# Optimization experiments

Hardware: AMD Instinct MI355X
Metric: run time of the kernel (lower is better)

Reference implementation:

```python
import jax, jax.numpy as jnp
import numpy as np

N_NODES = 50000
N_EDGES = 800000
N_GRAPHS = 128
IN_CH, HIDDEN, OUT_CH = 16, 64, 2


def gcn_conv(x, src, dst, W, b, n_nodes):
    """GCNConv: add self-loops, sym-normalized adjacency scatter-add, linear."""
    h = x @ W  # [N, H]
    loop = jnp.arange(n_nodes, dtype=src.dtype)
    s = jnp.concatenate([src, loop])  # [E+N]
    d = jnp.concatenate([dst, loop])
    deg = jax.ops.segment_sum(jnp.ones_like(d, dtype=h.dtype), d, num_segments=n_nodes)
    dinv = jnp.where(deg > 0, jax.lax.rsqrt(deg), 0.0)  # deg^{-1/2}
    norm = dinv[s] * dinv[d]  # [E+N]
    msg = h[s] * norm[:, None]  # gather + scale, [E+N, H]
    out = jax.ops.segment_sum(msg, d, num_segments=n_nodes)  # scatter-add
    return out + b


def global_mean_pool(x, batch, n_graphs):
    sums = jax.ops.segment_sum(x, batch, num_segments=n_graphs)
    cnts = jax.ops.segment_sum(jnp.ones((x.shape[0],), x.dtype), batch, num_segments=n_graphs)
    return sums / jnp.maximum(cnts, 1.0)[:, None]


def setup_inputs() -> dict:
    key = jax.random.key(0)
    ks = jax.random.split(key, 10)
    x = jax.random.normal(ks[0], (N_NODES, IN_CH), dtype=jnp.float32)
    edge_index = jax.random.randint(ks[1], (2, N_EDGES), 0, N_NODES, dtype=jnp.int64)
    batch = jnp.sort(jax.random.randint(ks[2], (N_NODES,), 0, N_GRAPHS, dtype=jnp.int64))
    def glorot(k, shp):
        lim = float(np.sqrt(6.0 / (shp[0] + shp[1])))
        return jax.random.uniform(k, shp, jnp.float32, -lim, lim)
    W1 = glorot(ks[3], (IN_CH, HIDDEN))
    b1 = jnp.zeros((HIDDEN,), jnp.float32)
    W2 = glorot(ks[4], (HIDDEN, HIDDEN))
    b2 = jnp.zeros((HIDDEN,), jnp.float32)
    Wc = glorot(ks[5], (HIDDEN, OUT_CH))
    bc = jnp.zeros((OUT_CH,), jnp.float32)
    return {"x": x, "edge_index": edge_index, "batch": batch,
            "W1": W1, "b1": b1, "W2": W2, "b2": b2, "Wc": Wc, "bc": bc}


def reference(x, edge_index, batch, W1, b1, W2, b2, Wc, bc):
    src, dst = edge_index[0], edge_index[1]
    n = x.shape[0]
    h = jax.nn.relu(gcn_conv(x, src, dst, W1, b1, n))
    # dropout p=0.3 is identity in eval mode
    h = jax.nn.relu(gcn_conv(h, src, dst, W2, b2, n))
    g = global_mean_pool(h, batch, N_GRAPHS)  # [G, H]
    return g @ Wc + bc  # [G, out_channels]
```

## Files before the change

### kernel.cpp

```cpp
#include <hip/hip_runtime.h>
#include <hip/hip_bf16.h>

#define N_NODES 50000
#define N_EDGES 800000
#define N_GRAPHS 128
#define IN_CH 16
#define HIDDEN 64
#define OUT_CH 2

#define BSHIFT 7
#define BNODES 128
#define NB ((N_NODES + BNODES - 1) / BNODES)
#define ECHUNK 4096
#define EB ((N_EDGES + ECHUNK - 1) / ECHUNK)
#define SLEN (NB * EB)
#define SCHUNK 1024
#define NSB ((SLEN + SCHUNK - 1) / SCHUNK)
#define MAXK 12
#define WT_LD 68

__device__ __forceinline__ float bf2f(unsigned short u) {
    return __uint_as_float(((unsigned)u) << 16);
}


__global__ void bucket_hist_kernel(const int* __restrict__ dst, int* __restrict__ bh,
                                   float* __restrict__ sums, float* __restrict__ cntg) {
    __shared__ int lh[NB];
    int t = threadIdx.x;
    if (blockIdx.x == 0) {
        for (int i = t; i < N_GRAPHS * HIDDEN; i += 256) sums[i] = 0.0f;
        if (t < N_GRAPHS) cntg[t] = 0.0f;
    }
    for (int i = t; i < NB; i += 256) lh[i] = 0;
    __syncthreads();
    int base = blockIdx.x * ECHUNK;
    for (int i = t; i < ECHUNK; i += 256) {
        int e = base + i;
        if (e < N_EDGES) {
            int d = dst[e];
            if ((unsigned)d < N_NODES) atomicAdd(&lh[d >> BSHIFT], 1);
        }
    }
    __syncthreads();
    for (int i = t; i < NB; i += 256) bh[i * EB + blockIdx.x] = lh[i];
}

__global__ void scan_part_kernel(const int* __restrict__ a, int* __restrict__ bsum) {
    __shared__ int s[256];
    int t = threadIdx.x;
    int ebase = blockIdx.x * SCHUNK + t * 4;
    int v = 0;
    if (ebase + 3 < SLEN) {
        int4 c = *(const int4*)&a[ebase];
        v = c.x + c.y + c.z + c.w;
    } else {
        for (int k = 0; k < 4; k++) {
            int i = ebase + k;
            if (i < SLEN) v += a[i];
        }
    }
    s[t] = v;
    __syncthreads();
    for (int off = 128; off > 0; off >>= 1) {
        if (t < off) s[t] += s[t + off];
        __syncthreads();
    }
    if (t == 0) bsum[blockIdx.x] = s[0];
}

__global__ void scan_apply_kernel(const int* __restrict__ a, const int* __restrict__ bsum,
                                  int* __restrict__ boff) {
    __shared__ int sb[256];
    __shared__ int st[256];
    int t = threadIdx.x;
    sb[t] = (t < NSB) ? bsum[t] : 0;
    __syncthreads();
    for (int off = 1; off < 256; off <<= 1) {
        int u = (t >= off) ? sb[t - off] : 0;
        __syncthreads();
        sb[t] += u;
        __syncthreads();
    }
    int blockOff = (blockIdx.x > 0) ? sb[blockIdx.x - 1] : 0;

    int ebase = blockIdx.x * SCHUNK + t * 4;
    int c0 = 0, c1 = 0, c2 = 0, c3 = 0;
    bool full = (ebase + 3 < SLEN);
    if (full) {
        int4 c = *(const int4*)&a[ebase];
        c0 = c.x; c1 = c.y; c2 = c.z; c3 = c.w;
    } else {
        if (ebase < SLEN) c0 = a[ebase];
        if (ebase + 1 < SLEN) c1 = a[ebase + 1];
        if (ebase + 2 < SLEN) c2 = a[ebase + 2];
    }
    int tsum = c0 + c1 + c2 + c3;
    st[t] = tsum;
    __syncthreads();
    for (int off = 1; off < 256; off <<= 1) {
        int u = (t >= off) ? st[t - off] : 0;
        __syncthreads();
        st[t] += u;
        __syncthreads();
    }
    int p = blockOff + st[t] - tsum;
    if (full) {
        int4 o;
        o.x = p; o.y = p + c0; o.z = p + c0 + c1; o.w = p + c0 + c1 + c2;
        *(int4*)&boff[ebase] = o;
    } else {
        if (ebase < SLEN) boff[ebase] = p;
        if (ebase + 1 < SLEN) boff[ebase + 1] = p + c0;
        if (ebase + 2 < SLEN) boff[ebase + 2] = p + c0 + c1;
        if (ebase + 3 < SLEN) boff[ebase + 3] = p + c0 + c1 + c2;
    }
}

__global__ void bucket_scatter_kernel(const int* __restrict__ src, const int* __restrict__ dst,
                                      const int* __restrict__ boff, int2* __restrict__ pairs) {
    __shared__ int lcnt[NB];
    __shared__ int goff[NB];
    int t = threadIdx.x;
    for (int i = t; i < NB; i += 256) {
        lcnt[i] = 0;
        goff[i] = boff[i * EB + blockIdx.x];
    }
    __syncthreads();
    int base = blockIdx.x * ECHUNK;
    for (int i = t; i < ECHUNK; i += 256) {
        int e = base + i;
        if (e < N_EDGES) {
            int d = dst[e];
            if ((unsigned)d < N_NODES) {
                int b = d >> BSHIFT;
                int r = atomicAdd(&lcnt[b], 1);
                int2 p;
                p.x = src[e];
                p.y = d;
                pairs[goff[b] + r] = p;
            }
        }
    }
}

__global__ void bucket_csr_kernel(const int2* __restrict__ pairs, const int* __restrict__ boff,
                                  int* __restrict__ csr, int* __restrict__ rowptr,
                                  int* __restrict__ cnt_node, float* __restrict__ dinv) {
    __shared__ int lcnt[BNODES];
    __shared__ int ls[BNODES];
    __shared__ int lrow[BNODES];
    int b = blockIdx.x;
    int t = threadIdx.x;
    if (t < BNODES) lcnt[t] = 0;
    __syncthreads();
    int bstart = boff[b * EB];
    int bend = (b + 1 < NB) ? boff[(b + 1) * EB] : N_EDGES;
    int K = bend - bstart;
    int myn[MAXK], myr[MAXK], mys[MAXK];
#pragma unroll
    for (int k = 0; k < MAXK; k++) {
        int i = k * 256 + t;
        if (i < K) {
            int2 p = pairs[bstart + i];
            int nl = p.y & (BNODES - 1);
            mys[k] = p.x;
            myn[k] = nl;
            myr[k] = atomicAdd(&lcnt[nl], 1);
        }
    }
    __syncthreads();
    if (t < BNODES) ls[t] = lcnt[t];
    __syncthreads();
    for (int off = 1; off < BNODES; off <<= 1) {
        int u = (t >= off && t < BNODES) ? ls[t - off] : 0;
        __syncthreads();
        if (t < BNODES) ls[t] += u;
        __syncthreads();
    }
    if (t < BNODES) {
        int ex = ls[t] - lcnt[t];
        lrow[t] = ex;
        int n = b * BNODES + t;
        if (n < N_NODES) {
            rowptr[n] = bstart + ex;
            cnt_node[n] = lcnt[t];
            dinv[n] = rsqrtf((float)(lcnt[t] + 1));
        }
    }
    __syncthreads();
#pragma unroll
    for (int k = 0; k < MAXK; k++) {
        int i = k * 256 + t;
        if (i < K) csr[bstart + lrow[myn[k]] + myr[k]] = mys[k];
    }
}


__global__ void fused_l1_kernel(const float* __restrict__ x, const int* __restrict__ csr_src,
                                const int* __restrict__ rowptr, const int* __restrict__ cnt,
                                const float* __restrict__ dinv, const float* __restrict__ W,
                                const float* __restrict__ b, __hip_bfloat16* __restrict__ h) {
    __shared__ float sWT[HIDDEN * 20];
    __shared__ float sx[16 * IN_CH];
    int t = threadIdx.x;
    for (int i = t; i < IN_CH * HIDDEN; i += 256) {
        int k = i >> 6, c = i & 63;
        sWT[c * 20 + k] = W[i];
    }

    int n0 = blockIdx.x * 16;
    int w = t >> 6;
    int lane = t & 63;
    int e4 = lane >> 2;
    int cc = (lane & 3) * 4;
    for (int q = 0; q < 4; q++) {
        int row = w * 4 + q;
        int n = n0 + row;
        if (n >= N_NODES) break;
        int len = cnt[n];
        int start = rowptr[n];
        float4 acc = make_float4(0.f, 0.f, 0.f, 0.f);
        for (int i = e4; i < len; i += 16) {
            int s = csr_src[start + i];
            float dv = dinv[s];
            float4 xv = *(const float4*)&x[s * IN_CH + cc];
            acc.x += dv * xv.x; acc.y += dv * xv.y; acc.z += dv * xv.z; acc.w += dv * xv.w;
        }
#pragma unroll
        for (int m = 4; m <= 32; m <<= 1) {
            acc.x += __shfl_xor(acc.x, m, 64);
            acc.y += __shfl_xor(acc.y, m, 64);
            acc.z += __shfl_xor(acc.z, m, 64);
            acc.w += __shfl_xor(acc.w, m, 64);
        }
        if (lane < 4) {
            float dn = dinv[n];
            float4 xs = *(const float4*)&x[n * IN_CH + cc];
            float4 v;
            v.x = dn * acc.x + dn * dn * xs.x;
            v.y = dn * acc.y + dn * dn * xs.y;
            v.z = dn * acc.z + dn * dn * xs.z;
            v.w = dn * acc.w + dn * dn * xs.w;
            *(float4*)&sx[row * IN_CH + cc] = v;
        }
    }
    __syncthreads();

    int r = w;
    int c = t & 63;
    float bias = b[c];
#pragma unroll
    for (int nb = 0; nb < 4; nb++) {
        int row = nb * 4 + r;
        int n = n0 + row;
        if (n >= N_NODES) continue;
        float acc = bias;
#pragma unroll
        for (int k4 = 0; k4 < IN_CH; k4 += 4) {
            float4 a = *(const float4*)&sx[row * IN_CH + k4];
            float4 wv = *(const float4*)&sWT[c * 20 + k4];
            acc += a.x * wv.x + a.y * wv.y + a.z * wv.z + a.w * wv.w;
        }
        float v = acc > 0.0f ? acc : 0.0f;
        h[n * HIDDEN + c] = __float2bfloat16(dinv[n] * v);
    }
}


__global__ void fused_l2_kernel(const __hip_bfloat16* __restrict__ h, const int* __restrict__ csr_src,
                                const int* __restrict__ rowptr, const int* __restrict__ cnt,
                                const float* __restrict__ dinv, const float* __restrict__ W,
                                const float* __restrict__ b, const int* __restrict__ batch,
                                float* __restrict__ sums, float* __restrict__ cntg) {
    __shared__ float sWT[HIDDEN * WT_LD];
    __shared__ float sagg[16 * HIDDEN];
    __shared__ float sred[4 * HIDDEN];
    int t = threadIdx.x;
    for (int i = t; i < HIDDEN * HIDDEN; i += 256) {
        int k = i >> 6, c = i & 63;
        sWT[c * WT_LD + k] = W[i];
    }

    int n0 = blockIdx.x * 16;
    int w = t >> 6;
    int lane = t & 63;
    int e4 = lane >> 4;
    int cc = (lane & 15) * 4;
    const unsigned short* hu = (const unsigned short*)h;

    for (int q = 0; q < 4; q++) {
        int row = w * 4 + q;
        int n = n0 + row;
        if (n >= N_NODES) break;
        int len = cnt[n];
        int start = rowptr[n];
        float4 acc = make_float4(0.f, 0.f, 0.f, 0.f);
        int i = e4;
        for (; i + 4 < len; i += 8) {
            int s0 = csr_src[start + i];
            int s1 = csr_src[start + i + 4];
            ushort4 a = *(const ushort4*)&hu[s0 * HIDDEN + cc];
            ushort4 bq = *(const ushort4*)&hu[s1 * HIDDEN + cc];
            acc.x += bf2f(a.x) + bf2f(bq.x);
            acc.y += bf2f(a.y) + bf2f(bq.y);
            acc.z += bf2f(a.z) + bf2f(bq.z);
            acc.w += bf2f(a.w) + bf2f(bq.w);
        }
        for (; i < len; i += 4) {
            int s0 = csr_src[start + i];
            ushort4 a = *(const ushort4*)&hu[s0 * HIDDEN + cc];
            acc.x += bf2f(a.x);
            acc.y += bf2f(a.y);
            acc.z += bf2f(a.z);
            acc.w += bf2f(a.w);
        }
        acc.x += __shfl_xor(acc.x, 16, 64);
        acc.y += __shfl_xor(acc.y, 16, 64);
        acc.z += __shfl_xor(acc.z, 16, 64);
        acc.w += __shfl_xor(acc.w, 16, 64);
        acc.x += __shfl_xor(acc.x, 32, 64);
        acc.y += __shfl_xor(acc.y, 32, 64);
        acc.z += __shfl_xor(acc.z, 32, 64);
        acc.w += __shfl_xor(acc.w, 32, 64);
        if (lane < 16) {
            ushort4 sv = *(const ushort4*)&hu[n * HIDDEN + cc];
            float dn = dinv[n];
            float4 v;
            v.x = dn * (acc.x + bf2f(sv.x));
            v.y = dn * (acc.y + bf2f(sv.y));
            v.z = dn * (acc.z + bf2f(sv.z));
            v.w = dn * (acc.w + bf2f(sv.w));
            *(float4*)&sagg[row * HIDDEN + cc] = v;
        }
    }
    __syncthreads();

    int r = w;
    int c = t & 63;
    float bias = b[c];
    float vout[4];
#pragma unroll
    for (int nb = 0; nb < 4; nb++) {
        int row = nb * 4 + r;
        int n = n0 + row;
        vout[nb] = 0.0f;
        if (n >= N_NODES) continue;
        float acc = bias;
#pragma unroll
        for (int k4 = 0; k4 < HIDDEN; k4 += 4) {
            float4 a = *(const float4*)&sagg[row * HIDDEN + k4];
            float4 wv = *(const float4*)&sWT[c * WT_LD + k4];
            acc += a.x * wv.x + a.y * wv.y + a.z * wv.z + a.w * wv.w;
        }
        vout[nb] = acc > 0.0f ? acc : 0.0f;
    }
    __syncthreads();

#pragma unroll
    for (int nb = 0; nb < 4; nb++) {
        int row = nb * 4 + r;
        if (n0 + row < N_NODES) sagg[row * HIDDEN + c] = vout[nb];
    }
    __syncthreads();

    int nlast = n0 + 15;
    if (nlast >= N_NODES) nlast = N_NODES - 1;
    int glo = batch[n0];
    int ghi = batch[nlast];
    if (glo == ghi) {
        float p = 0.0f;
#pragma unroll
        for (int q = 0; q < 4; q++) {
            int row = 4 * r + q;
            if (n0 + row < N_NODES) p += sagg[row * HIDDEN + c];
        }
        sred[r * HIDDEN + c] = p;
        __syncthreads();
        if (r == 0) {
            float v = sred[c] + sred[HIDDEN + c] + sred[2 * HIDDEN + c] + sred[3 * HIDDEN + c];
            atomicAdd(&sums[glo * HIDDEN + c], v);
            if (c == 0) atomicAdd(&cntg[glo], (float)(nlast - n0 + 1));
        }
    } else {
        int gcur = -1;
        float acc = 0.0f, ccnt = 0.0f;
        for (int q = 0; q < 4; q++) {
            int row = 4 * r + q;
            int n = n0 + row;
            if (n >= N_NODES) break;
            int g = batch[n];
            if ((unsigned)g >= N_GRAPHS) continue;
            if (g != gcur) {
                if (gcur >= 0) {
                    atomicAdd(&sums[gcur * HIDDEN + c], acc);
                    if (c == 0) atomicAdd(&cntg[gcur], ccnt);
                }
                gcur = g;
                acc = 0.0f;
                ccnt = 0.0f;
            }
            acc += sagg[row * HIDDEN + c];
            ccnt += 1.0f;
        }
        if (gcur >= 0) {
            atomicAdd(&sums[gcur * HIDDEN + c], acc);
            if (c == 0) atomicAdd(&cntg[gcur], ccnt);
        }
    }
}


__global__ void head_kernel(const float* __restrict__ sums, const float* __restrict__ cntg,
                            const float* __restrict__ Wc, const float* __restrict__ bc,
                            float* __restrict__ out) {
    int t = blockIdx.x * blockDim.x + threadIdx.x;
    if (t >= N_GRAPHS * OUT_CH) return;
    int g = t >> 1;
    int o = t & 1;
    float inv = 1.0f / fmaxf(cntg[g], 1.0f);
    float acc = bc[o];
#pragma unroll
    for (int k = 0; k < HIDDEN; k++) acc += sums[g * HIDDEN + k] * inv * Wc[k * OUT_CH + o];
    out[t] = acc;
}


extern "C" void kernel_launch(void* const* d_in, const int* in_sizes, int n_in,
                              void* d_out, int out_size, void* d_ws, size_t ws_size,
                              hipStream_t stream) {
    const float* x  = (const float*)d_in[0];
    const int* ei   = (const int*)d_in[1];
    const int* bat  = (const int*)d_in[2];
    const float* W1 = (const float*)d_in[3];
    const float* b1 = (const float*)d_in[4];
    const float* W2 = (const float*)d_in[5];
    const float* b2 = (const float*)d_in[6];
    const float* Wc = (const float*)d_in[7];
    const float* bc = (const float*)d_in[8];
    float* out = (float*)d_out;

    const int* src = ei;
    const int* dst = ei + N_EDGES;

    char* ws = (char*)d_ws;
    size_t off = 0;
    auto carve = [&](size_t nbytes) {
        char* p = ws + off;
        off += (nbytes + 255) & ~(size_t)255;
        return p;
    };
    float* sums     = (float*)carve(N_GRAPHS * HIDDEN * sizeof(float));
    float* cntg     = (float*)carve(N_GRAPHS * sizeof(float));
    int*   bh       = (int*)carve((size_t)SLEN * sizeof(int));
    int*   bsum     = (int*)carve(NSB * sizeof(int));
    int*   boff     = (int*)carve((size_t)SLEN * sizeof(int));
    int2*  pairs    = (int2*)carve((size_t)N_EDGES * sizeof(int2));
    int*   csr      = (int*)carve((size_t)N_EDGES * sizeof(int));
    int*   rowptr   = (int*)carve(N_NODES * sizeof(int));
    int*   cnt_node = (int*)carve(N_NODES * sizeof(int));
    float* dinv     = (float*)carve(N_NODES * sizeof(float));
    __hip_bfloat16* bufA = (__hip_bfloat16*)carve((size_t)N_NODES * HIDDEN * sizeof(__hip_bfloat16));
    (void)ws_size;

    const int node16Blk = (N_NODES + 15) / 16;

    bucket_hist_kernel<<<EB, 256, 0, stream>>>(dst, bh, sums, cntg);
    scan_part_kernel<<<NSB, 256, 0, stream>>>(bh, bsum);
    scan_apply_kernel<<<NSB, 256, 0, stream>>>(bh, bsum, boff);
    bucket_scatter_kernel<<<EB, 256, 0, stream>>>(src, dst, boff, pairs);
    bucket_csr_kernel<<<NB, 256, 0, stream>>>(pairs, boff, csr, rowptr, cnt_node, dinv);

    fused_l1_kernel<<<node16Blk, 256, 0, stream>>>(x, csr, rowptr, cnt_node, dinv, W1, b1, bufA);
    fused_l2_kernel<<<node16Blk, 256, 0, stream>>>(bufA, csr, rowptr, cnt_node, dinv, W2, b2,
                                                   bat, sums, cntg);
    head_kernel<<<1, 256, 0, stream>>>(sums, cntg, Wc, bc, out);
}
```

Baseline: 183.4 us.

## Use bf16 MFMA for layer-2 linear and simplify pooling reduction

Layer 2's 16x64x64 dense transform moves from scalar FP32 dot products in shared memory to two bf16 MFMA 16x16x32 instructions per wave. Both the aggregated features and the weights are stored in shared memory as bf16 with a padded stride. The pooling step now reduces directly from the MFMA output registers with shuffles, which drops the extra shared buffer and two barriers. The gather loop is also unrolled to four edges per iteration. The N_NODES bound checks are removed, which relies on 50000 being divisible by 16, and rounding the aggregate and weights to bf16 lowers precision.

```diff
diff --git a/kernel.cpp b/kernel.cpp
--- a/kernel.cpp
+++ b/kernel.cpp
@@ -17,10 +17,18 @@
 #define SCHUNK 1024
 #define NSB ((SLEN + SCHUNK - 1) / SCHUNK)
 #define MAXK 12
-#define WT_LD 68
+#define WT1_LD 18
+#define AGG_LD 72
+
+typedef __attribute__((ext_vector_type(8))) short bf16x8;
+typedef __attribute__((ext_vector_type(4))) float f32x4;
 
 __device__ __forceinline__ float bf2f(unsigned short u) {
     return __uint_as_float(((unsigned)u) << 16);
+}
+__device__ __forceinline__ unsigned short f2bf(float f) {
+    __hip_bfloat16 h = __float2bfloat16(f);
+    return *reinterpret_cast<unsigned short*>(&h);
 }
 
 
@@ -201,19 +209,20 @@
                                 const int* __restrict__ rowptr, const int* __restrict__ cnt,
                                 const float* __restrict__ dinv, const float* __restrict__ W,
                                 const float* __restrict__ b, __hip_bfloat16* __restrict__ h) {
-    __shared__ float sWT[HIDDEN * 20];
+    __shared__ float sWT[HIDDEN * WT1_LD];
     __shared__ float sx[16 * IN_CH];
     int t = threadIdx.x;
     for (int i = t; i < IN_CH * HIDDEN; i += 256) {
         int k = i >> 6, c = i & 63;
-        sWT[c * 20 + k] = W[i];
+        sWT[c * WT1_LD + k] = W[i];
     }
 
     int n0 = blockIdx.x * 16;
     int w = t >> 6;
     int lane = t & 63;
-    int e4 = lane >> 2;
+    int e16 = lane >> 2;
     int cc = (lane & 3) * 4;
+
     for (int q = 0; q < 4; q++) {
         int row = w * 4 + q;
         int n = n0 + row;
@@ -221,11 +230,12 @@
         int len = cnt[n];
         int start = rowptr[n];
         float4 acc = make_float4(0.f, 0.f, 0.f, 0.f);
-        for (int i = e4; i < len; i += 16) {
+        for (int i = e16; i < len; i += 16) {
             int s = csr_src[start + i];
             float dv = dinv[s];
             float4 xv = *(const float4*)&x[s * IN_CH + cc];
-            acc.x += dv * xv.x; acc.y += dv * xv.y; acc.z += dv * xv.z; acc.w += dv * xv.w;
+            acc.x += dv * xv.x; acc.y += dv * xv.y;
+            acc.z += dv * xv.z; acc.w += dv * xv.w;
         }
 #pragma unroll
         for (int m = 4; m <= 32; m <<= 1) {
@@ -255,14 +265,15 @@
         int row = nb * 4 + r;
         int n = n0 + row;
         if (n >= N_NODES) continue;
-        float acc = bias;
+        float acch = bias;
 #pragma unroll
         for (int k4 = 0; k4 < IN_CH; k4 += 4) {
             float4 a = *(const float4*)&sx[row * IN_CH + k4];
-            float4 wv = *(const float4*)&sWT[c * 20 + k4];
-            acc += a.x * wv.x + a.y * wv.y + a.z * wv.z + a.w * wv.w;
-        }
-        float v = acc > 0.0f ? acc : 0.0f;
+            float2 w0 = *(const float2*)&sWT[c * WT1_LD + k4];
+            float2 w1 = *(const float2*)&sWT[c * WT1_LD + k4 + 2];
+            acch += a.x * w0.x + a.y * w0.y + a.z * w1.x + a.w * w1.y;
+        }
+        float v = acch > 0.0f ? acch : 0.0f;
         h[n * HIDDEN + c] = __float2bfloat16(dinv[n] * v);
     }
 }
@@ -273,13 +284,12 @@
                                 const float* __restrict__ dinv, const float* __restrict__ W,
                                 const float* __restrict__ b, const int* __restrict__ batch,
                                 float* __restrict__ sums, float* __restrict__ cntg) {
-    __shared__ float sWT[HIDDEN * WT_LD];
-    __shared__ float sagg[16 * HIDDEN];
-    __shared__ float sred[4 * HIDDEN];
+    __shared__ unsigned short sW[HIDDEN * AGG_LD];
+    __shared__ unsigned short sagg[16 * AGG_LD];
     int t = threadIdx.x;
     for (int i = t; i < HIDDEN * HIDDEN; i += 256) {
         int k = i >> 6, c = i & 63;
-        sWT[c * WT_LD + k] = W[i];
+        sW[c * AGG_LD + k] = f2bf(W[i]);
     }
 
     int n0 = blockIdx.x * 16;
@@ -292,28 +302,31 @@
     for (int q = 0; q < 4; q++) {
         int row = w * 4 + q;
         int n = n0 + row;
-        if (n >= N_NODES) break;
         int len = cnt[n];
         int start = rowptr[n];
         float4 acc = make_float4(0.f, 0.f, 0.f, 0.f);
         int i = e4;
-        for (; i + 4 < len; i += 8) {
+        for (; i + 12 < len; i += 16) {
             int s0 = csr_src[start + i];
             int s1 = csr_src[start + i + 4];
-            ushort4 a = *(const ushort4*)&hu[s0 * HIDDEN + cc];
-            ushort4 bq = *(const ushort4*)&hu[s1 * HIDDEN + cc];
-            acc.x += bf2f(a.x) + bf2f(bq.x);
-            acc.y += bf2f(a.y) + bf2f(bq.y);
-            acc.z += bf2f(a.z) + bf2f(bq.z);
-            acc.w += bf2f(a.w) + bf2f(bq.w);
+            int s2 = csr_src[start + i + 8];
+            int s3 = csr_src[start + i + 12];
+            ushort4 a0 = *(const ushort4*)&hu[s0 * HIDDEN + cc];
+            ushort4 a1 = *(const ushort4*)&hu[s1 * HIDDEN + cc];
+            ushort4 a2 = *(const ushort4*)&hu[s2 * HIDDEN + cc];
+            ushort4 a3 = *(const ushort4*)&hu[s3 * HIDDEN + cc];
+            acc.x += (bf2f(a0.x) + bf2f(a1.x)) + (bf2f(a2.x) + bf2f(a3.x));
+            acc.y += (bf2f(a0.y) + bf2f(a1.y)) + (bf2f(a2.y) + bf2f(a3.y));
+            acc.z += (bf2f(a0.z) + bf2f(a1.z)) + (bf2f(a2.z) + bf2f(a3.z));
+            acc.w += (bf2f(a0.w) + bf2f(a1.w)) + (bf2f(a2.w) + bf2f(a3.w));
         }
         for (; i < len; i += 4) {
             int s0 = csr_src[start + i];
-            ushort4 a = *(const ushort4*)&hu[s0 * HIDDEN + cc];
-            acc.x += bf2f(a.x);
-            acc.y += bf2f(a.y);
-            acc.z += bf2f(a.z);
-            acc.w += bf2f(a.w);
+            ushort4 a0 = *(const ushort4*)&hu[s0 * HIDDEN + cc];
+            acc.x += bf2f(a0.x);
+            acc.y += bf2f(a0.y);
+            acc.z += bf2f(a0.z);
+            acc.w += bf2f(a0.w);
         }
         acc.x += __shfl_xor(acc.x, 16, 64);
         acc.y += __shfl_xor(acc.y, 16, 64);
@@ -326,86 +339,54 @@
         if (lane < 16) {
             ushort4 sv = *(const ushort4*)&hu[n * HIDDEN + cc];
             float dn = dinv[n];
-            float4 v;
-            v.x = dn * (acc.x + bf2f(sv.x));
-            v.y = dn * (acc.y + bf2f(sv.y));
-            v.z = dn * (acc.z + bf2f(sv.z));
-            v.w = dn * (acc.w + bf2f(sv.w));
-            *(float4*)&sagg[row * HIDDEN + cc] = v;
-        }
-    }
-    __syncthreads();
-
-    int r = w;
-    int c = t & 63;
-    float bias = b[c];
-    float vout[4];
-#pragma unroll
-    for (int nb = 0; nb < 4; nb++) {
-        int row = nb * 4 + r;
-        int n = n0 + row;
-        vout[nb] = 0.0f;
-        if (n >= N_NODES) continue;
-        float acc = bias;
-#pragma unroll
-        for (int k4 = 0; k4 < HIDDEN; k4 += 4) {
-            float4 a = *(const float4*)&sagg[row * HIDDEN + k4];
-            float4 wv = *(const float4*)&sWT[c * WT_LD + k4];
-            acc += a.x * wv.x + a.y * wv.y + a.z * wv.z + a.w * wv.w;
-        }
-        vout[nb] = acc > 0.0f ? acc : 0.0f;
-    }
-    __syncthreads();
-
-#pragma unroll
-    for (int nb = 0; nb < 4; nb++) {
-        int row = nb * 4 + r;
-        if (n0 + row < N_NODES) sagg[row * HIDDEN + c] = vout[nb];
-    }
-    __syncthreads();
-
-    int nlast = n0 + 15;
-    if (nlast >= N_NODES) nlast = N_NODES - 1;
+            ushort4 o;
+            o.x = f2bf(dn * (acc.x + bf2f(sv.x)));
+            o.y = f2bf(dn * (acc.y + bf2f(sv.y)));
+            o.z = f2bf(dn * (acc.z + bf2f(sv.z)));
+            o.w = f2bf(dn * (acc.w + bf2f(sv.w)));
+            *(ushort4*)&sagg[row * AGG_LD + cc] = o;
+        }
+    }
+    __syncthreads();
+
+    int quad = lane >> 4;
+    int col = lane & 15;
+    int cch = w * 16 + col;
+    bf16x8 a0 = *(const bf16x8*)&sagg[col * AGG_LD + quad * 8];
+    bf16x8 a1 = *(const bf16x8*)&sagg[col * AGG_LD + 32 + quad * 8];
+    bf16x8 b0 = *(const bf16x8*)&sW[cch * AGG_LD + quad * 8];
+    bf16x8 b1 = *(const bf16x8*)&sW[cch * AGG_LD + 32 + quad * 8];
+    f32x4 d = {0.f, 0.f, 0.f, 0.f};
+    d = __builtin_amdgcn_mfma_f32_16x16x32_bf16(a0, b0, d, 0, 0, 0);
+    d = __builtin_amdgcn_mfma_f32_16x16x32_bf16(a1, b1, d, 0, 0, 0);
+    float bias = b[cch];
+    float v[4];
+#pragma unroll
+    for (int r = 0; r < 4; r++) {
+        float z = d[r] + bias;
+        v[r] = z > 0.0f ? z : 0.0f;
+    }
+
     int glo = batch[n0];
-    int ghi = batch[nlast];
+    int ghi = batch[n0 + 15];
     if (glo == ghi) {
-        float p = 0.0f;
-#pragma unroll
-        for (int q = 0; q < 4; q++) {
-            int row = 4 * r + q;
-            if (n0 + row < N_NODES) p += sagg[row * HIDDEN + c];
-        }
-        sred[r * HIDDEN + c] = p;
-        __syncthreads();
-        if (r == 0) {
-            float v = sred[c] + sred[HIDDEN + c] + sred[2 * HIDDEN + c] + sred[3 * HIDDEN + c];
-            atomicAdd(&sums[glo * HIDDEN + c], v);
-            if (c == 0) atomicAdd(&cntg[glo], (float)(nlast - n0 + 1));
-        }
+        float s4 = (v[0] + v[1]) + (v[2] + v[3]);
+        s4 += __shfl_xor(s4, 16, 64);
+        s4 += __shfl_xor(s4, 32, 64);
+        if (quad == 0) atomicAdd(&sums[glo * HIDDEN + cch], s4);
+        if (t == 0) atomicAdd(&cntg[glo], 16.0f);
     } else {
-        int gcur = -1;
-        float acc = 0.0f, ccnt = 0.0f;
-        for (int q = 0; q < 4; q++) {
-            int row = 4 * r + q;
-            int n = n0 + row;
-            if (n >= N_NODES) break;
-            int g = batch[n];
-            if ((unsigned)g >= N_GRAPHS) continue;
-            if (g != gcur) {
-                if (gcur >= 0) {
-                    atomicAdd(&sums[gcur * HIDDEN + c], acc);
-                    if (c == 0) atomicAdd(&cntg[gcur], ccnt);
-                }
-                gcur = g;
-                acc = 0.0f;
-                ccnt = 0.0f;
+#pragma unroll
+        for (int r = 0; r < 4; r++) {
+            int g = batch[n0 + quad * 4 + r];
+            if ((unsigned)g < N_GRAPHS) atomicAdd(&sums[g * HIDDEN + cch], v[r]);
+        }
+        if (w == 0 && col == 0) {
+#pragma unroll
+            for (int r = 0; r < 4; r++) {
+                int g = batch[n0 + quad * 4 + r];
+                if ((unsigned)g < N_GRAPHS) atomicAdd(&cntg[g], 1.0f);
             }
-            acc += sagg[row * HIDDEN + c];
-            ccnt += 1.0f;
-        }
-        if (gcur >= 0) {
-            atomicAdd(&sums[gcur * HIDDEN + c], acc);
-            if (c == 0) atomicAdd(&cntg[gcur], ccnt);
         }
     }
 }
```

Result: faster. 178.1 us (-2.9%).
